# Kernel tuning notes

Hardware: AMD Instinct MI355X
Metric: run time of the kernel (lower is better)

## Reference

```python
import jax, jax.numpy as jnp
import numpy as np

L = 3        # number of GatedGCN layers
N = 30000    # nodes
E = 480000   # edges (avg degree 16)
D = 128      # hidden dim (= in_dim = out_dim)
IN = 128     # input feature dim
G = 64       # graphs in batch
C = 10       # classes


def setup_inputs() -> dict:
    key = jax.random.key(0)
    ks = jax.random.split(key, 32)
    s = 0.05  # weight scale to keep activations / sigmoid gates in a sane range
    inp = {
        "h": jax.random.normal(ks[0], (N, IN), jnp.float32),
        "e": jax.random.normal(ks[1], (E, IN), jnp.float32),
        "snorm_n": jax.random.uniform(ks[2], (N, 1), jnp.float32),
        "snorm_e": jax.random.uniform(ks[3], (E, 1), jnp.float32),
        "src": jax.random.randint(ks[4], (E,), 0, N, jnp.int32),
        "dst": jax.random.randint(ks[5], (E,), 0, N, jnp.int32),
        "graph_id": jnp.sort(jax.random.randint(ks[6], (N,), 0, G, jnp.int32)),
        # input embeddings
        "Wh_emb": jax.random.normal(ks[7], (IN, D), jnp.float32) * s,
        "bh_emb": jnp.zeros((D,), jnp.float32),
        "We_emb": jax.random.normal(ks[8], (IN, D), jnp.float32) * s,
        "be_emb": jnp.zeros((D,), jnp.float32),
        # per-layer A,B,C,D,E linears (stacked over L)
        "WA": jax.random.normal(ks[9], (L, D, D), jnp.float32) * s,
        "bA": jnp.zeros((L, D), jnp.float32),
        "WB": jax.random.normal(ks[10], (L, D, D), jnp.float32) * s,
        "bB": jnp.zeros((L, D), jnp.float32),
        "WC": jax.random.normal(ks[11], (L, D, D), jnp.float32) * s,
        "bC": jnp.zeros((L, D), jnp.float32),
        "WD": jax.random.normal(ks[12], (L, D, D), jnp.float32) * s,
        "bD": jnp.zeros((L, D), jnp.float32),
        "WE": jax.random.normal(ks[13], (L, D, D), jnp.float32) * s,
        "bE": jnp.zeros((L, D), jnp.float32),
        # batch-norm affine params (node / edge)
        "gn_h": jnp.ones((L, D), jnp.float32),
        "bt_h": jnp.zeros((L, D), jnp.float32),
        "gn_e": jnp.ones((L, D), jnp.float32),
        "bt_e": jnp.zeros((L, D), jnp.float32),
        # readout linear
        "Wr": jax.random.normal(ks[14], (D, C), jnp.float32) * s,
        "br": jnp.zeros((C,), jnp.float32),
    }
    return inp


def _bn(x, gamma, beta):
    # training-mode BatchNorm1d: biased batch stats over the node/edge axis
    mu = jnp.mean(x, axis=0)
    var = jnp.var(x, axis=0)
    return (x - mu) * jax.lax.rsqrt(var + 1e-5) * gamma + beta


def reference(h, e, snorm_n, snorm_e, src, dst, graph_id,
              Wh_emb, bh_emb, We_emb, be_emb,
              WA, bA, WB, bB, WC, bC, WD, bD, WE, bE,
              gn_h, bt_h, gn_e, bt_e, Wr, br):
    n_nodes = h.shape[0]
    h = h @ Wh_emb + bh_emb
    e = e @ We_emb + be_emb
    for l in range(WA.shape[0]):
        h_in, e_in = h, e
        Ah = h @ WA[l] + bA[l]
        Bh = h @ WB[l] + bB[l]
        Dh = h @ WD[l] + bD[l]
        Eh = h @ WE[l] + bE[l]
        Ce = e @ WC[l] + bC[l]
        # message: e_ij = Ce + Dh_src + Eh_dst ; gate = sigmoid(e_ij)
        e_new = Ce + Dh[src] + Eh[dst]                       # [E, D]
        sig = jax.nn.sigmoid(e_new)
        # reduce at dst: gated weighted mean of Bh_src
        num = jax.ops.segment_sum(sig * Bh[src], dst, num_segments=n_nodes)
        den = jax.ops.segment_sum(sig, dst, num_segments=n_nodes)
        h_new = Ah + num / (den + 1e-6)
        # graph norm
        h_new = h_new * snorm_n
        e_new = e_new * snorm_e
        # batch norm + ReLU + residual (dropout p=0 -> identity)
        h_new = jax.nn.relu(_bn(h_new, gn_h[l], bt_h[l]))
        e_new = jax.nn.relu(_bn(e_new, gn_e[l], bt_e[l]))
        h = h_in + h_new
        e = e_in + e_new
    # mean_nodes readout per graph, then linear classifier
    sums = jax.ops.segment_sum(h, graph_id, num_segments=G)
    cnt = jax.ops.segment_sum(jnp.ones((n_nodes, 1), h.dtype), graph_id, num_segments=G)
    hg = sums / jnp.maximum(cnt, 1.0)
    return hg @ Wr + br
```

## Files before the change

kernel.cpp:

```cpp
#include <hip/hip_runtime.h>
#include <cstdint>
#include <cstddef>

#define N_NODES  30000
#define N_EDGES  480000
#define N_LAYERS 3
#define N_GRAPHS 64
#define N_CLASS  10
#define NREP     32

typedef __attribute__((ext_vector_type(8))) short short8v;
typedef __attribute__((ext_vector_type(4))) float f32x4;

__device__ __forceinline__ unsigned short f2bf(float x) {
  union { float f; unsigned u; } v; v.f = x;
  unsigned r = v.u + 0x7FFFu + ((v.u >> 16) & 1u);
  return (unsigned short)(r >> 16);
}
__device__ __forceinline__ float bf2f(unsigned short h) {
  union { unsigned u; float f; } v; v.u = ((unsigned)h) << 16;
  return v.f;
}
__device__ __forceinline__ int swzW(int row, int off16) {
  return (row << 8) | (off16 ^ ((row & 7) << 4));
}

__global__ void wconv(const float* __restrict__ Wh, const float* __restrict__ We,
                      const float* __restrict__ WA, const float* __restrict__ WB,
                      const float* __restrict__ WC, const float* __restrict__ WD,
                      const float* __restrict__ WE, unsigned short* __restrict__ Wt)
{
  const int mi  = blockIdx.x >> 6;
  const int idx = (blockIdx.x & 63) * 256 + threadIdx.x;
  const float* src;
  if      (mi == 0) src = Wh;
  else if (mi == 1) src = We;
  else if (mi < 5)  src = WA + (size_t)(mi - 2) * 16384;
  else if (mi < 8)  src = WB + (size_t)(mi - 5) * 16384;
  else if (mi < 11) src = WC + (size_t)(mi - 8) * 16384;
  else if (mi < 14) src = WD + (size_t)(mi - 11) * 16384;
  else              src = WE + (size_t)(mi - 14) * 16384;
  const int k = idx >> 7, n = idx & 127;
  Wt[(size_t)mi * 16384 + (size_t)n * 128 + k] = f2bf(src[idx]);
}

struct GemmArgs {
  const unsigned short* Wt[4];
  const float* bias[4];
  unsigned short* out[4];
};

template<int NMAT, bool AFP32, bool APPLY>
__global__ __launch_bounds__(256)
void gemm_mm(const void* __restrict__ Ap, GemmArgs g, int M,
             const unsigned short* __restrict__ tb, const float2* __restrict__ pqh,
             unsigned short* __restrict__ hout)
{
  __shared__ __align__(16) unsigned char WL[32768];
  unsigned short* Wl = (unsigned short*)WL;
  const int t = threadIdx.x;
  const int w = t >> 6, l = t & 63;
  const int lr = l & 15, lkb = (l >> 4) * 8;
  const int r0 = blockIdx.x * 64;
  const bool vrow = (r0 + w * 16 + lr) < M;
  int arow = r0 + w * 16 + lr; if (arow >= M) arow = M - 1;

  short8v a[4];
  if (AFP32) {
    const float* A = (const float*)Ap;
#pragma unroll
    for (int kk = 0; kk < 4; ++kk) {
      const float* p = A + (size_t)arow * 128 + kk * 32 + lkb;
      const float4 u = *(const float4*)p;
      const float4 v = *(const float4*)(p + 4);
      short8v av;
      av[0]=f2bf(u.x); av[1]=f2bf(u.y); av[2]=f2bf(u.z); av[3]=f2bf(u.w);
      av[4]=f2bf(v.x); av[5]=f2bf(v.y); av[6]=f2bf(v.z); av[7]=f2bf(v.w);
      a[kk] = av;
    }
  } else if (APPLY) {
    const unsigned short* A = (const unsigned short*)Ap;
#pragma unroll
    for (int kk = 0; kk < 4; ++kk) {
      const short8v tv = *(const short8v*)(tb + (size_t)arow * 128 + kk * 32 + lkb);
      const short8v hr = *(const short8v*)(A + (size_t)arow * 128 + kk * 32 + lkb);
      short8v av;
#pragma unroll
      for (int j = 0; j < 8; ++j) {
        const float2 PQ = pqh[kk * 32 + lkb + j];
        const float x = bf2f((unsigned short)tv[j]) * PQ.x + PQ.y;
        av[j] = (short)f2bf(bf2f((unsigned short)hr[j]) + fmaxf(x, 0.f));
      }
      a[kk] = av;
      if (vrow) *(short8v*)(hout + (size_t)arow * 128 + kk * 32 + lkb) = av;
    }
  } else {
    const unsigned short* A = (const unsigned short*)Ap;
#pragma unroll
    for (int kk = 0; kk < 4; ++kk)
      a[kk] = *(const short8v*)(A + (size_t)arow * 128 + kk * 32 + lkb);
  }

#pragma unroll
  for (int m = 0; m < NMAT; ++m) {
    if (m) __syncthreads();
#pragma unroll
    for (int p = 0; p < 8; ++p) {
      const int ci = t + p * 256;
      *(short8v*)(WL + swzW(ci >> 4, (ci & 15) * 16)) = *(const short8v*)(g.Wt[m] + (size_t)ci * 8);
    }
    __syncthreads();
    f32x4 acc[8];
#pragma unroll
    for (int ct = 0; ct < 8; ++ct) acc[ct] = (f32x4){0.f, 0.f, 0.f, 0.f};
#pragma unroll
    for (int kk = 0; kk < 4; ++kk)
#pragma unroll
      for (int ct = 0; ct < 8; ++ct) {
        const short8v b = *(const short8v*)(WL + swzW(ct * 16 + lr, kk * 64 + (l >> 4) * 16));
        acc[ct] = __builtin_amdgcn_mfma_f32_16x16x32_bf16(a[kk], b, acc[ct], 0, 0, 0);
      }
    __syncthreads();
#pragma unroll
    for (int ct = 0; ct < 8; ++ct) {
      const float bb = g.bias[m][ct * 16 + lr];
#pragma unroll
      for (int q = 0; q < 4; ++q)
        Wl[(w * 16 + (l >> 4) * 4 + q) * 136 + ct * 16 + lr] = f2bf(acc[ct][q] + bb);
    }
    __syncthreads();
    unsigned short* out = g.out[m];
#pragma unroll
    for (int p = 0; p < 4; ++p) {
      const int ci = t + p * 256;
      const int rr = ci >> 4, co = (ci & 15) * 8;
      const int grow = r0 + rr;
      if (grow < M)
        *(short8v*)(out + (size_t)grow * 128 + co) = *(const short8v*)(Wl + rr * 136 + co);
    }
  }
}

template<int LMODE>
__global__ __launch_bounds__(256)
void edge_kern(const void* __restrict__ Ap, unsigned short* __restrict__ eres,
               unsigned short* __restrict__ enew,
               const unsigned short* __restrict__ Wt, const float* __restrict__ bias,
               const unsigned short* __restrict__ Dh, const unsigned short* __restrict__ Eh,
               const int* __restrict__ src, const int* __restrict__ dst,
               const float* __restrict__ snorm_e, const float2* __restrict__ pq)
{
  __shared__ __align__(16) unsigned char SM[32768];
  __shared__ float2 pql[128];
  unsigned short* TB = (unsigned short*)SM;
  const int t = threadIdx.x;
  const int w = t >> 6, l = t & 63;
  const int lr = l & 15, lkb = (l >> 4) * 8;
  const int r0 = blockIdx.x * 64;
  const int arow = r0 + w * 16 + lr;
  if (LMODE >= 2 && t < 128) pql[t] = pq[t];
#pragma unroll
  for (int p = 0; p < 8; ++p) {
    const int ci = t + p * 256;
    *(short8v*)(SM + swzW(ci >> 4, (ci & 15) * 16)) = *(const short8v*)(Wt + (size_t)ci * 8);
  }

  short8v a[4];
  if (LMODE == 0) {
    const float* A = (const float*)Ap;
#pragma unroll
    for (int kk = 0; kk < 4; ++kk) {
      const float* p2 = A + (size_t)arow * 128 + kk * 32 + lkb;
      const float4 u = *(const float4*)p2;
      const float4 v = *(const float4*)(p2 + 4);
      short8v av;
      av[0]=f2bf(u.x); av[1]=f2bf(u.y); av[2]=f2bf(u.z); av[3]=f2bf(u.w);
      av[4]=f2bf(v.x); av[5]=f2bf(v.y); av[6]=f2bf(v.z); av[7]=f2bf(v.w);
      a[kk] = av;
    }
  } else if (LMODE == 1) {
    const unsigned short* A = (const unsigned short*)Ap;
#pragma unroll
    for (int kk = 0; kk < 4; ++kk)
      a[kk] = *(const short8v*)(A + (size_t)arow * 128 + kk * 32 + lkb);
  }
  __syncthreads();

  if (LMODE >= 2) {
    const unsigned short* A = (const unsigned short*)Ap;
    const float sn = snorm_e[arow];
#pragma unroll
    for (int kk = 0; kk < 4; ++kk) {
      const short8v ep = *(const short8v*)(enew + (size_t)arow * 128 + kk * 32 + lkb);
      const short8v er = *(const short8v*)(A + (size_t)arow * 128 + kk * 32 + lkb);
      short8v av;
#pragma unroll
      for (int j = 0; j < 8; ++j) {
        const float2 PQ = pql[kk * 32 + lkb + j];
        const float x = bf2f((unsigned short)ep[j]) * sn * PQ.x + PQ.y;
        av[j] = (short)f2bf(bf2f((unsigned short)er[j]) + fmaxf(x, 0.f));
      }
      a[kk] = av;
      if (LMODE == 2)
        *(short8v*)(eres + (size_t)arow * 128 + kk * 32 + lkb) = av;
    }
  }

  f32x4 acc[8];
#pragma unroll
  for (int ct = 0; ct < 8; ++ct) acc[ct] = (f32x4){0.f, 0.f, 0.f, 0.f};
#pragma unroll
  for (int kk = 0; kk < 4; ++kk)
#pragma unroll
    for (int ct = 0; ct < 8; ++ct) {
      const short8v b = *(const short8v*)(SM + swzW(ct * 16 + lr, kk * 64 + (l >> 4) * 16));
      acc[ct] = __builtin_amdgcn_mfma_f32_16x16x32_bf16(a[kk], b, acc[ct], 0, 0, 0);
    }
  __syncthreads();
#pragma unroll
  for (int ct = 0; ct < 8; ++ct) {
    const float bb = bias[ct * 16 + lr];
#pragma unroll
    for (int q = 0; q < 4; ++q)
      TB[(w * 16 + (l >> 4) * 4 + q) * 132 + ct * 16 + lr] = f2bf(acc[ct][q] + bb);
  }
  __syncthreads();
#pragma unroll
  for (int p = 0; p < 4; ++p) {
    const int ci = t + p * 256;
    const int rr = ci >> 4, co = (ci & 15) * 8;
    const int edge = r0 + rr;
    const short8v ce = *(const short8v*)(TB + rr * 132 + co);
    if (LMODE == 0) {
      *(short8v*)(eres + (size_t)edge * 128 + co) = ce;
    } else {
      const int s = src[edge], d = dst[edge];
      const short8v dv = *(const short8v*)(Dh + (size_t)s * 128 + co);
      const short8v ev = *(const short8v*)(Eh + (size_t)d * 128 + co);
      short8v ov;
#pragma unroll
      for (int j = 0; j < 8; ++j)
        ov[j] = (short)f2bf(bf2f((unsigned short)ce[j]) + bf2f((unsigned short)dv[j]) + bf2f((unsigned short)ev[j]));
      *(short8v*)(enew + (size_t)edge * 128 + co) = ov;
    }
  }
}

__global__ void hist_kernel(const int* __restrict__ dst, int* __restrict__ cnt, int E)
{
  const int i = blockIdx.x * 256 + threadIdx.x;
  if (i < E) atomicAdd(&cnt[dst[i]], 1);
}

__global__ void scan_kernel(const int* __restrict__ cnt, int* __restrict__ start,
                            int* __restrict__ cursor, int n, int total)
{
  __shared__ int lds[1024];
  const int tid = threadIdx.x;
  const int chunk = (n + 1023) / 1024;
  const int lo = tid * chunk, hi = min(lo + chunk, n);
  int s = 0;
  for (int i = lo; i < hi; ++i) s += cnt[i];
  lds[tid] = s;
  __syncthreads();
  for (int off = 1; off < 1024; off <<= 1) {
    const int v = (tid >= off) ? lds[tid - off] : 0;
    __syncthreads();
    lds[tid] += v;
    __syncthreads();
  }
  int run = (tid == 0) ? 0 : lds[tid - 1];
  for (int i = lo; i < hi; ++i) { start[i] = run; cursor[i] = run; run += cnt[i]; }
  if (tid == 0) start[n] = total;
}

__global__ void scatter_kernel(const int* __restrict__ dst, const int* __restrict__ src,
                               const float* __restrict__ sne, int* __restrict__ cursor,
                               int* __restrict__ csr, int* __restrict__ csrc,
                               float* __restrict__ csne, int E)
{
  const int i = blockIdx.x * 256 + threadIdx.x;
  if (i < E) {
    const int p = atomicAdd(&cursor[dst[i]], 1);
    csr[p] = i; csrc[p] = src[i]; csne[p] = sne[i];
  }
}

__global__ __launch_bounds__(256)
void aggregate(const unsigned short* __restrict__ enew, const unsigned short* __restrict__ Bh,
               const unsigned short* __restrict__ Ah, const float* __restrict__ snorm_n,
               const int* __restrict__ start, const int* __restrict__ csr,
               const int* __restrict__ csrc, const float* __restrict__ csne,
               unsigned short* __restrict__ tbuf, float* __restrict__ statrep, int doE)
{
  __shared__ float2 red[16][132];
  const int t = threadIdx.x;
  const int g = t >> 4, q = t & 15;
  const int v = blockIdx.x * 16 + g;
  const int s0 = start[v], s1 = start[v + 1];
  float num[8] = {0,0,0,0,0,0,0,0}, den[8] = {0,0,0,0,0,0,0,0};
  float psE[8] = {0,0,0,0,0,0,0,0}, pqE[8] = {0,0,0,0,0,0,0,0};

  float sn = 0.f;
  short8v ev = {}, bv = {};
  if (s0 < s1) {
    const int eid = csr[s0];
    sn = csne[s0];
    ev = *(const short8v*)(enew + (size_t)eid * 128 + q * 8);
    bv = *(const short8v*)(Bh + (size_t)csrc[s0] * 128 + q * 8);
  }
  for (int i = s0; i < s1; ++i) {
    float snn = 0.f;
    short8v evn = {}, bvn = {};
    if (i + 1 < s1) {
      const int eid = csr[i + 1];
      snn = csne[i + 1];
      evn = *(const short8v*)(enew + (size_t)eid * 128 + q * 8);
      bvn = *(const short8v*)(Bh + (size_t)csrc[i + 1] * 128 + q * 8);
    }
#pragma unroll
    for (int j = 0; j < 8; ++j) {
      const float en = bf2f((unsigned short)ev[j]);
      const float sg = 1.f / (1.f + __expf(-en));
      num[j] = fmaf(sg, bf2f((unsigned short)bv[j]), num[j]);
      den[j] += sg;
      if (doE) { const float tv = en * sn; psE[j] += tv; pqE[j] = fmaf(tv, tv, pqE[j]); }
    }
    ev = evn; bv = bvn; sn = snn;
  }
  const float snv = snorm_n[v];
  const short8v av = *(const short8v*)(Ah + (size_t)v * 128 + q * 8);
  float hv[8];
  short8v tout;
#pragma unroll
  for (int j = 0; j < 8; ++j) {
    hv[j] = (bf2f((unsigned short)av[j]) + num[j] / (den[j] + 1e-6f)) * snv;
    tout[j] = (short)f2bf(hv[j]);
  }
  *(short8v*)(tbuf + (size_t)v * 128 + q * 8) = tout;

  float* rep = statrep + (size_t)(blockIdx.x & (NREP - 1)) * 512;
#pragma unroll
  for (int j = 0; j < 8; ++j) red[g][q * 8 + j] = make_float2(hv[j], hv[j] * hv[j]);
  __syncthreads();
  if (t < 128) {
    float s = 0.f, qq = 0.f;
    for (int gg = 0; gg < 16; ++gg) { s += red[gg][t].x; qq += red[gg][t].y; }
    atomicAdd(rep + t, s); atomicAdd(rep + 128 + t, qq);
  }
  if (doE) {
    __syncthreads();
#pragma unroll
    for (int j = 0; j < 8; ++j) red[g][q * 8 + j] = make_float2(psE[j], pqE[j]);
    __syncthreads();
    if (t < 128) {
      float s = 0.f, qq = 0.f;
      for (int gg = 0; gg < 16; ++gg) { s += red[gg][t].x; qq += red[gg][t].y; }
      atomicAdd(rep + 256 + t, s); atomicAdd(rep + 384 + t, qq);
    }
  }
}

__global__ void finalize_kernel(float* __restrict__ rep, float2* __restrict__ pqh,
                                float2* __restrict__ pqe,
                                const float* __restrict__ gn_h_l, const float* __restrict__ bt_h_l,
                                const float* __restrict__ gn_e_l, const float* __restrict__ bt_e_l,
                                float invN, float invE, int doE)
{
  const int c = threadIdx.x;
  float sH = 0.f, qH = 0.f, sE = 0.f, qE = 0.f;
  for (int r = 0; r < NREP; ++r) {
    float* p = rep + (size_t)r * 512;
    sH += p[c]; qH += p[128 + c]; sE += p[256 + c]; qE += p[384 + c];
    p[c] = 0.f; p[128 + c] = 0.f; p[256 + c] = 0.f; p[384 + c] = 0.f;
  }
  const float muH = sH * invN;
  const float vH  = fmaxf(qH * invN - muH * muH, 0.f);
  const float PH  = rsqrtf(vH + 1e-5f) * gn_h_l[c];
  pqh[c] = make_float2(PH, bt_h_l[c] - muH * PH);
  if (doE) {
    const float muE = sE * invE;
    const float vE  = fmaxf(qE * invE - muE * muE, 0.f);
    const float PE  = rsqrtf(vE + 1e-5f) * gn_e_l[c];
    pqe[c] = make_float2(PE, bt_e_l[c] - muE * PE);
  }
}

__global__ void readout_scatter(const unsigned short* __restrict__ h, const unsigned short* __restrict__ tb,
                                const float2* __restrict__ pqh, const int* __restrict__ gid,
                                float* __restrict__ gsum, int* __restrict__ gcnt, int N)
{
  const int c = threadIdx.x;
  const float2 PQ = pqh[c];
  const int row0 = blockIdx.x * 256;
  int cur = -1, cnt = 0;
  float s = 0.f;
  for (int r = 0; r < 256; ++r) {
    const int v = row0 + r;
    if (v >= N) break;
    const int g = gid[v];
    if (g != cur) {
      if (cur >= 0) {
        atomicAdd(&gsum[(size_t)cur * 128 + c], s);
        if (c == 0) atomicAdd(&gcnt[cur], cnt);
      }
      cur = g; s = 0.f; cnt = 0;
    }
    s += bf2f(h[(size_t)v * 128 + c]) + fmaxf(bf2f(tb[(size_t)v * 128 + c]) * PQ.x + PQ.y, 0.f);
    ++cnt;
  }
  if (cur >= 0) {
    atomicAdd(&gsum[(size_t)cur * 128 + c], s);
    if (c == 0) atomicAdd(&gcnt[cur], cnt);
  }
}

__global__ void readout_final(const float* __restrict__ gsum, const int* __restrict__ gcnt,
                              const float* __restrict__ Wr, const float* __restrict__ br,
                              float* __restrict__ out)
{
  const int g = blockIdx.x;
  const int t = threadIdx.x;
  __shared__ float hg[128];
  const float cnt = fmaxf((float)gcnt[g], 1.f);
  hg[t] = gsum[(size_t)g * 128 + t] / cnt;
  __syncthreads();
  if (t < N_CLASS) {
    float acc = br[t];
    for (int k = 0; k < 128; ++k) acc = fmaf(hg[k], Wr[k * N_CLASS + t], acc);
    out[g * N_CLASS + t] = acc;
  }
}

extern "C" void kernel_launch(void* const* d_in, const int* in_sizes, int n_in,
                              void* d_out, int out_size, void* d_ws, size_t ws_size,
                              hipStream_t stream)
{
  const float* h_in    = (const float*)d_in[0];
  const float* e_in    = (const float*)d_in[1];
  const float* snorm_n = (const float*)d_in[2];
  const float* snorm_e = (const float*)d_in[3];
  const int*   src     = (const int*)d_in[4];
  const int*   dst     = (const int*)d_in[5];
  const int*   gid     = (const int*)d_in[6];
  const float* Wh_emb  = (const float*)d_in[7];
  const float* bh_emb  = (const float*)d_in[8];
  const float* We_emb  = (const float*)d_in[9];
  const float* be_emb  = (const float*)d_in[10];
  const float* WA = (const float*)d_in[11]; const float* bA = (const float*)d_in[12];
  const float* WB = (const float*)d_in[13]; const float* bB = (const float*)d_in[14];
  const float* WC = (const float*)d_in[15]; const float* bC = (const float*)d_in[16];
  const float* WD = (const float*)d_in[17]; const float* bD = (const float*)d_in[18];
  const float* WE = (const float*)d_in[19]; const float* bE = (const float*)d_in[20];
  const float* gn_h = (const float*)d_in[21]; const float* bt_h = (const float*)d_in[22];
  const float* gn_e = (const float*)d_in[23]; const float* bt_e = (const float*)d_in[24];
  const float* Wr = (const float*)d_in[25]; const float* br = (const float*)d_in[26];
  float* out = (float*)d_out;
  (void)in_sizes; (void)n_in; (void)out_size; (void)ws_size;

  char* ws = (char*)d_ws;
  size_t off = 0;
  auto alloc = [&](size_t bytes) -> char* {
    off = (off + 255) & ~(size_t)255;
    char* p = ws + off;
    off += bytes;
    return p;
  };
  const size_t ND = (size_t)N_NODES * 128, ED = (size_t)N_EDGES * 128;
  unsigned short* hbuf = (unsigned short*)alloc(ND * 2);
  unsigned short* ebuf = (unsigned short*)alloc(ED * 2);
  unsigned short* enew = (unsigned short*)alloc(ED * 2);
  unsigned short* Ah   = (unsigned short*)alloc(ND * 2);
  unsigned short* Bh   = (unsigned short*)alloc(ND * 2);
  unsigned short* Dh   = (unsigned short*)alloc(ND * 2);
  unsigned short* Eh   = (unsigned short*)alloc(ND * 2);
  unsigned short* tbuf = (unsigned short*)alloc(ND * 2);
  unsigned short* Wt   = (unsigned short*)alloc((size_t)17 * 16384 * 2);
  float2* pqh          = (float2*)alloc(128 * 8);
  float2* pqe          = (float2*)alloc(128 * 8);
  int* start  = (int*)alloc((size_t)(N_NODES + 1) * 4);
  int* cursor = (int*)alloc((size_t)N_NODES * 4);
  int* csr    = (int*)alloc((size_t)N_EDGES * 4);
  int* csrc   = (int*)alloc((size_t)N_EDGES * 4);
  float* csne = (float*)alloc((size_t)N_EDGES * 4);
  char* zbase = (char*)alloc(0);
  int*   cnt     = (int*)alloc((size_t)N_NODES * 4);
  float* statrep = (float*)alloc((size_t)NREP * 512 * 4);
  float* gsum    = (float*)alloc((size_t)N_GRAPHS * 128 * 4);
  int*   gcnt    = (int*)alloc((size_t)N_GRAPHS * 4);
  char* zend = (char*)alloc(0);

  hipMemsetAsync(zbase, 0, (size_t)(zend - zbase), stream);

  wconv<<<17 * 64, 256, 0, stream>>>(Wh_emb, We_emb, WA, WB, WC, WD, WE, Wt);

  hist_kernel<<<(N_EDGES + 255) / 256, 256, 0, stream>>>(dst, cnt, N_EDGES);
  scan_kernel<<<1, 1024, 0, stream>>>(cnt, start, cursor, N_NODES, N_EDGES);
  scatter_kernel<<<(N_EDGES + 255) / 256, 256, 0, stream>>>(dst, src, snorm_e, cursor,
                                                            csr, csrc, csne, N_EDGES);

  const int gbN = (N_NODES + 63) / 64;
  const int gbE = N_EDGES / 64;

  {
    GemmArgs g{};
    g.Wt[0] = Wt + 0 * 16384; g.bias[0] = bh_emb; g.out[0] = hbuf;
    gemm_mm<1, true, false><<<gbN, 256, 0, stream>>>(h_in, g, N_NODES, nullptr, nullptr, nullptr);
  }
  edge_kern<0><<<gbE, 256, 0, stream>>>(e_in, ebuf, nullptr, Wt + 1 * 16384, be_emb,
                                        nullptr, nullptr, nullptr, nullptr, nullptr, nullptr);

  for (int l = 0; l < N_LAYERS; ++l) {
    const size_t bOff = (size_t)l * 128;
    const int doE = (l < N_LAYERS - 1) ? 1 : 0;
    {
      GemmArgs g{};
      g.Wt[0] = Wt + (size_t)(2 + l)  * 16384; g.bias[0] = bA + bOff; g.out[0] = Ah;
      g.Wt[1] = Wt + (size_t)(5 + l)  * 16384; g.bias[1] = bB + bOff; g.out[1] = Bh;
      g.Wt[2] = Wt + (size_t)(11 + l) * 16384; g.bias[2] = bD + bOff; g.out[2] = Dh;
      g.Wt[3] = Wt + (size_t)(14 + l) * 16384; g.bias[3] = bE + bOff; g.out[3] = Eh;
      if (l == 0)
        gemm_mm<4, false, false><<<gbN, 256, 0, stream>>>(hbuf, g, N_NODES, nullptr, nullptr, nullptr);
      else
        gemm_mm<4, false, true><<<gbN, 256, 0, stream>>>(hbuf, g, N_NODES, tbuf, pqh, hbuf);
    }
    const unsigned short* WtC = Wt + (size_t)(8 + l) * 16384;
    if (l == 0)
      edge_kern<1><<<gbE, 256, 0, stream>>>(ebuf, nullptr, enew, WtC, bC + bOff,
                                            Dh, Eh, src, dst, nullptr, nullptr);
    else if (l == 1)
      edge_kern<2><<<gbE, 256, 0, stream>>>(ebuf, ebuf, enew, WtC, bC + bOff,
                                            Dh, Eh, src, dst, snorm_e, pqe);
    else
      edge_kern<3><<<gbE, 256, 0, stream>>>(ebuf, nullptr, enew, WtC, bC + bOff,
                                            Dh, Eh, src, dst, snorm_e, pqe);
    aggregate<<<N_NODES / 16, 256, 0, stream>>>(enew, Bh, Ah, snorm_n, start, csr, csrc, csne,
                                                tbuf, statrep, doE);
    finalize_kernel<<<1, 128, 0, stream>>>(statrep, pqh, pqe, gn_h + bOff, bt_h + bOff,
                                           gn_e + bOff, bt_e + bOff,
                                           1.f / N_NODES, 1.f / N_EDGES, doE);
  }

  readout_scatter<<<(N_NODES + 255) / 256, 128, 0, stream>>>(hbuf, tbuf, pqh, gid, gsum, gcnt, N_NODES);
  readout_final<<<N_GRAPHS, 128, 0, stream>>>(gsum, gcnt, Wr, br, out);
}
```

Measured before the change: 935.7 us.

## Store edge data in dst-sorted CSR order and fuse embeddings into layer-0 kernels

Edges are now permuted into dst-sorted CSR order once, in the layer-0 edge kernel, which gathers e_in via csr. All later edge buffers (ebuf, enew, snorm_e) live in that sorted order, so aggregate reads enew contiguously instead of through an index. The node and edge embedding GEMMs are fused into the layer-0 node GEMM and edge kernels, which removes two launches and a round trip of hbuf/ebuf. The cost is one extra cdst array, a scattered fp32 gather of e_in, and more shared memory per edge block, which may lower occupancy.

```diff
diff --git a/kernel.cpp b/kernel.cpp
--- a/kernel.cpp
+++ b/kernel.cpp
@@ -50,11 +50,12 @@
   unsigned short* out[4];
 };
 
-template<int NMAT, bool AFP32, bool APPLY>
+template<int NMAT, int AMODE>
 __global__ __launch_bounds__(256)
 void gemm_mm(const void* __restrict__ Ap, GemmArgs g, int M,
              const unsigned short* __restrict__ tb, const float2* __restrict__ pqh,
-             unsigned short* __restrict__ hout)
+             unsigned short* __restrict__ hout,
+             const unsigned short* __restrict__ WtX, const float* __restrict__ biasX)
 {
   __shared__ __align__(16) unsigned char WL[32768];
   unsigned short* Wl = (unsigned short*)WL;
@@ -66,7 +67,12 @@
   int arow = r0 + w * 16 + lr; if (arow >= M) arow = M - 1;
 
   short8v a[4];
-  if (AFP32) {
+  if (AMODE == 2) {
+#pragma unroll
+    for (int p = 0; p < 8; ++p) {
+      const int ci = t + p * 256;
+      *(short8v*)(WL + swzW(ci >> 4, (ci & 15) * 16)) = *(const short8v*)(WtX + (size_t)ci * 8);
+    }
     const float* A = (const float*)Ap;
 #pragma unroll
     for (int kk = 0; kk < 4; ++kk) {
@@ -78,7 +84,32 @@
       av[4]=f2bf(v.x); av[5]=f2bf(v.y); av[6]=f2bf(v.z); av[7]=f2bf(v.w);
       a[kk] = av;
     }
-  } else if (APPLY) {
+    __syncthreads();
+    f32x4 acc[8];
+#pragma unroll
+    for (int ct = 0; ct < 8; ++ct) acc[ct] = (f32x4){0.f, 0.f, 0.f, 0.f};
+#pragma unroll
+    for (int kk = 0; kk < 4; ++kk)
+#pragma unroll
+      for (int ct = 0; ct < 8; ++ct) {
+        const short8v b = *(const short8v*)(WL + swzW(ct * 16 + lr, kk * 64 + (l >> 4) * 16));
+        acc[ct] = __builtin_amdgcn_mfma_f32_16x16x32_bf16(a[kk], b, acc[ct], 0, 0, 0);
+      }
+    __syncthreads();
+#pragma unroll
+    for (int ct = 0; ct < 8; ++ct) {
+      const float bb = biasX[ct * 16 + lr];
+#pragma unroll
+      for (int q = 0; q < 4; ++q)
+        Wl[(w * 16 + (l >> 4) * 4 + q) * 136 + ct * 16 + lr] = f2bf(acc[ct][q] + bb);
+    }
+    __syncthreads();
+#pragma unroll
+    for (int kk = 0; kk < 4; ++kk) {
+      a[kk] = *(const short8v*)(Wl + (w * 16 + lr) * 136 + kk * 32 + lkb);
+      if (vrow) *(short8v*)(hout + (size_t)arow * 128 + kk * 32 + lkb) = a[kk];
+    }
+  } else if (AMODE == 1) {
     const unsigned short* A = (const unsigned short*)Ap;
 #pragma unroll
     for (int kk = 0; kk < 4; ++kk) {
@@ -103,7 +134,7 @@
 
 #pragma unroll
   for (int m = 0; m < NMAT; ++m) {
-    if (m) __syncthreads();
+    if (m || AMODE == 2) __syncthreads();
 #pragma unroll
     for (int p = 0; p < 8; ++p) {
       const int ci = t + p * 256;
@@ -143,70 +174,106 @@
 
 template<int LMODE>
 __global__ __launch_bounds__(256)
-void edge_kern(const void* __restrict__ Ap, unsigned short* __restrict__ eres,
-               unsigned short* __restrict__ enew,
-               const unsigned short* __restrict__ Wt, const float* __restrict__ bias,
+void edge_kern(const float* __restrict__ e_in, const int* __restrict__ csr,
+               unsigned short* __restrict__ eres, unsigned short* __restrict__ enew,
+               const unsigned short* __restrict__ WtEmb, const float* __restrict__ bEmb,
+               const unsigned short* __restrict__ WtC, const float* __restrict__ bC,
                const unsigned short* __restrict__ Dh, const unsigned short* __restrict__ Eh,
-               const int* __restrict__ src, const int* __restrict__ dst,
-               const float* __restrict__ snorm_e, const float2* __restrict__ pq)
+               const int* __restrict__ csrc, const int* __restrict__ cdst,
+               const float* __restrict__ csne, const float2* __restrict__ pq)
 {
   __shared__ __align__(16) unsigned char SM[32768];
+  __shared__ __align__(16) unsigned short TB2[64 * 132];
   __shared__ float2 pql[128];
-  unsigned short* TB = (unsigned short*)SM;
   const int t = threadIdx.x;
   const int w = t >> 6, l = t & 63;
   const int lr = l & 15, lkb = (l >> 4) * 8;
   const int r0 = blockIdx.x * 64;
-  const int arow = r0 + w * 16 + lr;
-  if (LMODE >= 2 && t < 128) pql[t] = pq[t];
-#pragma unroll
-  for (int p = 0; p < 8; ++p) {
-    const int ci = t + p * 256;
-    *(short8v*)(SM + swzW(ci >> 4, (ci & 15) * 16)) = *(const short8v*)(Wt + (size_t)ci * 8);
-  }
+  const int pos = r0 + w * 16 + lr;
 
   short8v a[4];
+  f32x4 acc[8];
+
   if (LMODE == 0) {
-    const float* A = (const float*)Ap;
-#pragma unroll
-    for (int kk = 0; kk < 4; ++kk) {
-      const float* p2 = A + (size_t)arow * 128 + kk * 32 + lkb;
-      const float4 u = *(const float4*)p2;
-      const float4 v = *(const float4*)(p2 + 4);
+#pragma unroll
+    for (int p = 0; p < 8; ++p) {
+      const int ci = t + p * 256;
+      *(short8v*)(SM + swzW(ci >> 4, (ci & 15) * 16)) = *(const short8v*)(WtEmb + (size_t)ci * 8);
+    }
+#pragma unroll
+    for (int p = 0; p < 4; ++p) {
+      const int ci = t + p * 256;
+      const int rr = ci >> 4, co = (ci & 15) * 8;
+      const float* sp = e_in + (size_t)csr[r0 + rr] * 128 + co;
+      const float4 u = *(const float4*)sp;
+      const float4 v = *(const float4*)(sp + 4);
       short8v av;
       av[0]=f2bf(u.x); av[1]=f2bf(u.y); av[2]=f2bf(u.z); av[3]=f2bf(u.w);
       av[4]=f2bf(v.x); av[5]=f2bf(v.y); av[6]=f2bf(v.z); av[7]=f2bf(v.w);
-      a[kk] = av;
-    }
-  } else if (LMODE == 1) {
-    const unsigned short* A = (const unsigned short*)Ap;
+      *(short8v*)(TB2 + rr * 132 + co) = av;
+    }
+    __syncthreads();
 #pragma unroll
     for (int kk = 0; kk < 4; ++kk)
-      a[kk] = *(const short8v*)(A + (size_t)arow * 128 + kk * 32 + lkb);
-  }
-  __syncthreads();
-
-  if (LMODE >= 2) {
-    const unsigned short* A = (const unsigned short*)Ap;
-    const float sn = snorm_e[arow];
+      a[kk] = *(const short8v*)(TB2 + (w * 16 + lr) * 132 + kk * 32 + lkb);
+#pragma unroll
+    for (int ct = 0; ct < 8; ++ct) acc[ct] = (f32x4){0.f, 0.f, 0.f, 0.f};
+#pragma unroll
+    for (int kk = 0; kk < 4; ++kk)
+#pragma unroll
+      for (int ct = 0; ct < 8; ++ct) {
+        const short8v b = *(const short8v*)(SM + swzW(ct * 16 + lr, kk * 64 + (l >> 4) * 16));
+        acc[ct] = __builtin_amdgcn_mfma_f32_16x16x32_bf16(a[kk], b, acc[ct], 0, 0, 0);
+      }
+    __syncthreads();
+#pragma unroll
+    for (int ct = 0; ct < 8; ++ct) {
+      const float bb = bEmb[ct * 16 + lr];
+#pragma unroll
+      for (int q = 0; q < 4; ++q)
+        TB2[(w * 16 + (l >> 4) * 4 + q) * 132 + ct * 16 + lr] = f2bf(acc[ct][q] + bb);
+    }
+#pragma unroll
+    for (int p = 0; p < 8; ++p) {
+      const int ci = t + p * 256;
+      *(short8v*)(SM + swzW(ci >> 4, (ci & 15) * 16)) = *(const short8v*)(WtC + (size_t)ci * 8);
+    }
+    __syncthreads();
 #pragma unroll
     for (int kk = 0; kk < 4; ++kk) {
-      const short8v ep = *(const short8v*)(enew + (size_t)arow * 128 + kk * 32 + lkb);
-      const short8v er = *(const short8v*)(A + (size_t)arow * 128 + kk * 32 + lkb);
+      a[kk] = *(const short8v*)(TB2 + (w * 16 + lr) * 132 + kk * 32 + lkb);
+      *(short8v*)(eres + (size_t)pos * 128 + kk * 32 + lkb) = a[kk];
+    }
+  } else {
+    if (t < 128) pql[t] = pq[t];
+#pragma unroll
+    for (int p = 0; p < 8; ++p) {
+      const int ci = t + p * 256;
+      *(short8v*)(SM + swzW(ci >> 4, (ci & 15) * 16)) = *(const short8v*)(WtC + (size_t)ci * 8);
+    }
+    const float sn = csne[pos];
+    short8v ep[4], er[4];
+#pragma unroll
+    for (int kk = 0; kk < 4; ++kk) {
+      ep[kk] = *(const short8v*)(enew + (size_t)pos * 128 + kk * 32 + lkb);
+      er[kk] = *(const short8v*)(eres + (size_t)pos * 128 + kk * 32 + lkb);
+    }
+    __syncthreads();
+#pragma unroll
+    for (int kk = 0; kk < 4; ++kk) {
       short8v av;
 #pragma unroll
       for (int j = 0; j < 8; ++j) {
         const float2 PQ = pql[kk * 32 + lkb + j];
-        const float x = bf2f((unsigned short)ep[j]) * sn * PQ.x + PQ.y;
-        av[j] = (short)f2bf(bf2f((unsigned short)er[j]) + fmaxf(x, 0.f));
+        const float x = bf2f((unsigned short)ep[kk][j]) * sn * PQ.x + PQ.y;
+        av[j] = (short)f2bf(bf2f((unsigned short)er[kk][j]) + fmaxf(x, 0.f));
       }
       a[kk] = av;
       if (LMODE == 2)
-        *(short8v*)(eres + (size_t)arow * 128 + kk * 32 + lkb) = av;
-    }
-  }
-
-  f32x4 acc[8];
+        *(short8v*)(eres + (size_t)pos * 128 + kk * 32 + lkb) = av;
+    }
+  }
+
 #pragma unroll
   for (int ct = 0; ct < 8; ++ct) acc[ct] = (f32x4){0.f, 0.f, 0.f, 0.f};
 #pragma unroll
@@ -216,33 +283,29 @@
       const short8v b = *(const short8v*)(SM + swzW(ct * 16 + lr, kk * 64 + (l >> 4) * 16));
       acc[ct] = __builtin_amdgcn_mfma_f32_16x16x32_bf16(a[kk], b, acc[ct], 0, 0, 0);
     }
-  __syncthreads();
+  if (LMODE == 0) __syncthreads();
 #pragma unroll
   for (int ct = 0; ct < 8; ++ct) {
-    const float bb = bias[ct * 16 + lr];
+    const float bb = bC[ct * 16 + lr];
 #pragma unroll
     for (int q = 0; q < 4; ++q)
-      TB[(w * 16 + (l >> 4) * 4 + q) * 132 + ct * 16 + lr] = f2bf(acc[ct][q] + bb);
+      TB2[(w * 16 + (l >> 4) * 4 + q) * 132 + ct * 16 + lr] = f2bf(acc[ct][q] + bb);
   }
   __syncthreads();
 #pragma unroll
   for (int p = 0; p < 4; ++p) {
     const int ci = t + p * 256;
     const int rr = ci >> 4, co = (ci & 15) * 8;
-    const int edge = r0 + rr;
-    const short8v ce = *(const short8v*)(TB + rr * 132 + co);
-    if (LMODE == 0) {
-      *(short8v*)(eres + (size_t)edge * 128 + co) = ce;
-    } else {
-      const int s = src[edge], d = dst[edge];
-      const short8v dv = *(const short8v*)(Dh + (size_t)s * 128 + co);
-      const short8v ev = *(const short8v*)(Eh + (size_t)d * 128 + co);
-      short8v ov;
-#pragma unroll
-      for (int j = 0; j < 8; ++j)
-        ov[j] = (short)f2bf(bf2f((unsigned short)ce[j]) + bf2f((unsigned short)dv[j]) + bf2f((unsigned short)ev[j]));
-      *(short8v*)(enew + (size_t)edge * 128 + co) = ov;
-    }
+    const int pp = r0 + rr;
+    const int s = csrc[pp], d = cdst[pp];
+    const short8v ce = *(const short8v*)(TB2 + rr * 132 + co);
+    const short8v dv = *(const short8v*)(Dh + (size_t)s * 128 + co);
+    const short8v ev = *(const short8v*)(Eh + (size_t)d * 128 + co);
+    short8v ov;
+#pragma unroll
+    for (int j = 0; j < 8; ++j)
+      ov[j] = (short)f2bf(bf2f((unsigned short)ce[j]) + bf2f((unsigned short)dv[j]) + bf2f((unsigned short)ev[j]));
+    *(short8v*)(enew + (size_t)pp * 128 + co) = ov;
   }
 }
 
@@ -277,20 +340,20 @@
 __global__ void scatter_kernel(const int* __restrict__ dst, const int* __restrict__ src,
                                const float* __restrict__ sne, int* __restrict__ cursor,
                                int* __restrict__ csr, int* __restrict__ csrc,
-                               float* __restrict__ csne, int E)
+                               int* __restrict__ cdst, float* __restrict__ csne, int E)
 {
   const int i = blockIdx.x * 256 + threadIdx.x;
   if (i < E) {
     const int p = atomicAdd(&cursor[dst[i]], 1);
-    csr[p] = i; csrc[p] = src[i]; csne[p] = sne[i];
+    csr[p] = i; csrc[p] = src[i]; cdst[p] = dst[i]; csne[p] = sne[i];
   }
 }
 
 __global__ __launch_bounds__(256)
 void aggregate(const unsigned short* __restrict__ enew, const unsigned short* __restrict__ Bh,
                const unsigned short* __restrict__ Ah, const float* __restrict__ snorm_n,
-               const int* __restrict__ start, const int* __restrict__ csr,
-               const int* __restrict__ csrc, const float* __restrict__ csne,
+               const int* __restrict__ start, const int* __restrict__ csrc,
+               const float* __restrict__ csne,
                unsigned short* __restrict__ tbuf, float* __restrict__ statrep, int doE)
 {
   __shared__ float2 red[16][132];
@@ -304,18 +367,16 @@
   float sn = 0.f;
   short8v ev = {}, bv = {};
   if (s0 < s1) {
-    const int eid = csr[s0];
     sn = csne[s0];
-    ev = *(const short8v*)(enew + (size_t)eid * 128 + q * 8);
+    ev = *(const short8v*)(enew + (size_t)s0 * 128 + q * 8);
     bv = *(const short8v*)(Bh + (size_t)csrc[s0] * 128 + q * 8);
   }
   for (int i = s0; i < s1; ++i) {
     float snn = 0.f;
     short8v evn = {}, bvn = {};
     if (i + 1 < s1) {
-      const int eid = csr[i + 1];
       snn = csne[i + 1];
-      evn = *(const short8v*)(enew + (size_t)eid * 128 + q * 8);
+      evn = *(const short8v*)(enew + (size_t)(i + 1) * 128 + q * 8);
       bvn = *(const short8v*)(Bh + (size_t)csrc[i + 1] * 128 + q * 8);
     }
 #pragma unroll
@@ -482,6 +543,7 @@
   int* cursor = (int*)alloc((size_t)N_NODES * 4);
   int* csr    = (int*)alloc((size_t)N_EDGES * 4);
   int* csrc   = (int*)alloc((size_t)N_EDGES * 4);
+  int* cdst   = (int*)alloc((size_t)N_EDGES * 4);
   float* csne = (float*)alloc((size_t)N_EDGES * 4);
   char* zbase = (char*)alloc(0);
   int*   cnt     = (int*)alloc((size_t)N_NODES * 4);
@@ -497,18 +559,10 @@
   hist_kernel<<<(N_EDGES + 255) / 256, 256, 0, stream>>>(dst, cnt, N_EDGES);
   scan_kernel<<<1, 1024, 0, stream>>>(cnt, start, cursor, N_NODES, N_EDGES);
   scatter_kernel<<<(N_EDGES + 255) / 256, 256, 0, stream>>>(dst, src, snorm_e, cursor,
-                                                            csr, csrc, csne, N_EDGES);
+                                                            csr, csrc, cdst, csne, N_EDGES);
 
   const int gbN = (N_NODES + 63) / 64;
   const int gbE = N_EDGES / 64;
-
-  {
-    GemmArgs g{};
-    g.Wt[0] = Wt + 0 * 16384; g.bias[0] = bh_emb; g.out[0] = hbuf;
-    gemm_mm<1, true, false><<<gbN, 256, 0, stream>>>(h_in, g, N_NODES, nullptr, nullptr, nullptr);
-  }
-  edge_kern<0><<<gbE, 256, 0, stream>>>(e_in, ebuf, nullptr, Wt + 1 * 16384, be_emb,
-                                        nullptr, nullptr, nullptr, nullptr, nullptr, nullptr);
 
   for (int l = 0; l < N_LAYERS; ++l) {
     const size_t bOff = (size_t)l * 128;
@@ -520,21 +574,23 @@
       g.Wt[2] = Wt + (size_t)(11 + l) * 16384; g.bias[2] = bD + bOff; g.out[2] = Dh;
       g.Wt[3] = Wt + (size_t)(14 + l) * 16384; g.bias[3] = bE + bOff; g.out[3] = Eh;
       if (l == 0)
-        gemm_mm<4, false, false><<<gbN, 256, 0, stream>>>(hbuf, g, N_NODES, nullptr, nullptr, nullptr);
+        gemm_mm<4, 2><<<gbN, 256, 0, stream>>>(h_in, g, N_NODES, nullptr, nullptr, hbuf,
+                                               Wt + 0 * 16384, bh_emb);
       else
-        gemm_mm<4, false, true><<<gbN, 256, 0, stream>>>(hbuf, g, N_NODES, tbuf, pqh, hbuf);
+        gemm_mm<4, 1><<<gbN, 256, 0, stream>>>(hbuf, g, N_NODES, tbuf, pqh, hbuf,
+                                               nullptr, nullptr);
     }
     const unsigned short* WtC = Wt + (size_t)(8 + l) * 16384;
     if (l == 0)
-      edge_kern<1><<<gbE, 256, 0, stream>>>(ebuf, nullptr, enew, WtC, bC + bOff,
-                                            Dh, Eh, src, dst, nullptr, nullptr);
+      edge_kern<0><<<gbE, 256, 0, stream>>>(e_in, csr, ebuf, enew, Wt + 1 * 16384, be_emb,
+                                            WtC, bC + bOff, Dh, Eh, csrc, cdst, csne, nullptr);
     else if (l == 1)
-      edge_kern<2><<<gbE, 256, 0, stream>>>(ebuf, ebuf, enew, WtC, bC + bOff,
-                                            Dh, Eh, src, dst, snorm_e, pqe);
+      edge_kern<2><<<gbE, 256, 0, stream>>>(nullptr, nullptr, ebuf, enew, nullptr, nullptr,
+                                            WtC, bC + bOff, Dh, Eh, csrc, cdst, csne, pqe);
     else
-      edge_kern<3><<<gbE, 256, 0, stream>>>(ebuf, nullptr, enew, WtC, bC + bOff,
-                                            Dh, Eh, src, dst, snorm_e, pqe);
-    aggregate<<<N_NODES / 16, 256, 0, stream>>>(enew, Bh, Ah, snorm_n, start, csr, csrc, csne,
+      edge_kern<3><<<gbE, 256, 0, stream>>>(nullptr, nullptr, ebuf, enew, nullptr, nullptr,
+                                            WtC, bC + bOff, Dh, Eh, csrc, cdst, csne, pqe);
+    aggregate<<<N_NODES / 16, 256, 0, stream>>>(enew, Bh, Ah, snorm_n, start, csrc, csne,
                                                 tbuf, statrep, doE);
     finalize_kernel<<<1, 128, 0, stream>>>(statrep, pqh, pqe, gn_h + bOff, bt_h + bOff,
                                            gn_e + bOff, bt_e + bOff,
```

New measurement: 919.9 us. About the same (-1.7%).
